# Optimization experiments

Measured on AMD Instinct MI355X. Metric: run time of the kernel, lower is better.

## Reference

```python
import jax, jax.numpy as jnp
import numpy as np

N_NODES = 50000
EMBED_DIM = 512
N_EDGES = 800000
NEG_SLOPE = 0.01  # nn.LeakyReLU default


def setup_inputs() -> dict:
    key = jax.random.key(0)
    k1, k2, k3 = jax.random.split(key, 3)
    X = jax.random.normal(k1, (N_NODES, EMBED_DIM), dtype=jnp.float32)
    # Glorot-ish scale for the GCNConv weight
    W = jax.random.normal(k2, (EMBED_DIM, EMBED_DIM), dtype=jnp.float32) / np.sqrt(EMBED_DIM)
    b = jnp.zeros((EMBED_DIM,), dtype=jnp.float32)
    edge_index = jax.random.randint(k3, (2, N_EDGES), 0, N_NODES, dtype=jnp.int32)
    return {"X": X, "W": W, "b": b, "edge_index": edge_index}


def reference(X, W, b, edge_index):
    N = X.shape[0]
    # GCNConv: add self-loops, symmetric normalization deg^-1/2 A deg^-1/2
    loop = jnp.arange(N, dtype=edge_index.dtype)
    src = jnp.concatenate([edge_index[0], loop])  # [E+N]
    dst = jnp.concatenate([edge_index[1], loop])  # [E+N]
    deg = jax.ops.segment_sum(jnp.ones_like(dst, dtype=X.dtype), dst, num_segments=N)
    dinv = jnp.where(deg > 0, jax.lax.rsqrt(deg), 0.0)  # deg^{-1/2}, inf->0
    norm = dinv[src] * dinv[dst]                         # [E+N]
    H = X @ W                                            # [N, D] dense GEMM
    msgs = H[src] * norm[:, None]                        # [E+N, D] gathered messages
    out = jax.ops.segment_sum(msgs, dst, num_segments=N) + b
    # LeakyReLU activation; Dropout is identity in eval mode
    return jnp.where(out >= 0, out, NEG_SLOPE * out)
```

## Files before the change

kernel.cpp:

```cpp
#include <hip/hip_runtime.h>
#include <cstdint>
#include <cstddef>

#define DFEAT 512
#define BM 128
#define BN 128
#define BK 32

typedef __attribute__((ext_vector_type(8))) short bf16x8;
typedef __attribute__((ext_vector_type(4))) float f32x4;

#define GLOBAL_AS __attribute__((address_space(1)))
#define LDS_AS __attribute__((address_space(3)))

__device__ __forceinline__ unsigned short f2bf(float f) {
  unsigned u = __float_as_uint(f);
  u = u + 0x7fffu + ((u >> 16) & 1u);
  return (unsigned short)(u >> 16);
}

__device__ __forceinline__ float bf2f_lo(unsigned u) { return __uint_as_float(u << 16); }
__device__ __forceinline__ float bf2f_hi(unsigned u) { return __uint_as_float(u & 0xffff0000u); }

__device__ __forceinline__ void gl_lds16(const void* g, void* l) {
  __builtin_amdgcn_global_load_lds((const GLOBAL_AS unsigned int*)g,
                                   (LDS_AS unsigned int*)l, 16, 0, 0);
}

__global__ void k_init(int* __restrict__ deg, int* __restrict__ fill, int N) {
  int i = blockIdx.x * blockDim.x + threadIdx.x;
  if (i < N) { deg[i] = 1; fill[i] = 0; }
}

__global__ void k_count(const int* __restrict__ dst, int* __restrict__ deg, int E) {
  int i = blockIdx.x * blockDim.x + threadIdx.x;
  if (i < E) atomicAdd(&deg[dst[i]], 1);
}

__global__ void k_dinv(const int* __restrict__ deg, float* __restrict__ dinv, int N) {
  int i = blockIdx.x * blockDim.x + threadIdx.x;
  if (i < N) dinv[i] = rsqrtf((float)deg[i]);
}

__global__ void k_scan(const int* __restrict__ deg, int* __restrict__ rowStart, int N) {
  const int t = threadIdx.x;
  const int C = (N + 1023) / 1024;
  int lo = t * C;
  int hi = lo + C; if (hi > N) hi = N; if (lo > N) lo = N;
  int sum = 0;
  for (int i = lo; i < hi; ++i) sum += deg[i];
  __shared__ int sm[1024];
  sm[t] = sum;
  __syncthreads();
  for (int d = 1; d < 1024; d <<= 1) {
    int v = (t >= d) ? sm[t - d] : 0;
    __syncthreads();
    sm[t] += v;
    __syncthreads();
  }
  int off = sm[t] - sum;
  for (int i = lo; i < hi; ++i) { rowStart[i] = off; off += deg[i]; }
  if (t == 1023) rowStart[N] = sm[1023];
}

__global__ void k_fill(const int* __restrict__ src, const int* __restrict__ dst,
                       const int* __restrict__ rowStart, int* __restrict__ fill,
                       int2* __restrict__ cw, const float* __restrict__ dinv, int E, int N) {
  int i = blockIdx.x * blockDim.x + threadIdx.x;
  if (i >= E + N) return;
  int d, s;
  if (i < E) { d = dst[i]; s = src[i]; }
  else       { d = i - E; s = d; }
  int pos = rowStart[d] + atomicAdd(&fill[d], 1);
  int2 q; q.x = s; q.y = __float_as_int(dinv[s]);
  cw[pos] = q;
}

__global__ void k_wt(const float* __restrict__ W, unsigned short* __restrict__ Wt) {
  int i = blockIdx.x * blockDim.x + threadIdx.x;
  int k = i >> 9, n = i & 511;
  Wt[(size_t)n * DFEAT + k] = f2bf(W[i]);
}

__global__ void k_xb(const float* __restrict__ X, unsigned short* __restrict__ Xb, int total8) {
  int i = blockIdx.x * blockDim.x + threadIdx.x;
  if (i >= total8) return;
  const float4 a = *reinterpret_cast<const float4*>(X + (size_t)i * 8);
  const float4 c = *reinterpret_cast<const float4*>(X + (size_t)i * 8 + 4);
  uint4 o;
  o.x = (unsigned)f2bf(a.x) | ((unsigned)f2bf(a.y) << 16);
  o.y = (unsigned)f2bf(a.z) | ((unsigned)f2bf(a.w) << 16);
  o.z = (unsigned)f2bf(c.x) | ((unsigned)f2bf(c.y) << 16);
  o.w = (unsigned)f2bf(c.z) | ((unsigned)f2bf(c.w) << 16);
  *reinterpret_cast<uint4*>(Xb + (size_t)i * 8) = o;
}

__global__ __launch_bounds__(256) void k_aggregate(const unsigned short* __restrict__ Xb,
                                                   const int2* __restrict__ cw,
                                                   const int* __restrict__ rowStart,
                                                   const float* __restrict__ dinv,
                                                   unsigned short* __restrict__ Y, int N) {
  const int row = blockIdx.x * 4 + (threadIdx.x >> 6);
  const int lane = threadIdx.x & 63;
  float acc[8] = {0.f, 0.f, 0.f, 0.f, 0.f, 0.f, 0.f, 0.f};
  if (row < N) {
    const int s = rowStart[row], e = rowStart[row + 1];
    int p = s;
    for (; p + 4 <= e; p += 4) {
      const int2 q0 = cw[p + 0];
      const int2 q1 = cw[p + 1];
      const int2 q2 = cw[p + 2];
      const int2 q3 = cw[p + 3];
      const uint4 v0 = *reinterpret_cast<const uint4*>(Xb + (size_t)q0.x * DFEAT + lane * 8);
      const uint4 v1 = *reinterpret_cast<const uint4*>(Xb + (size_t)q1.x * DFEAT + lane * 8);
      const uint4 v2 = *reinterpret_cast<const uint4*>(Xb + (size_t)q2.x * DFEAT + lane * 8);
      const uint4 v3 = *reinterpret_cast<const uint4*>(Xb + (size_t)q3.x * DFEAT + lane * 8);
      const float w0 = __int_as_float(q0.y), w1 = __int_as_float(q1.y);
      const float w2 = __int_as_float(q2.y), w3 = __int_as_float(q3.y);
      acc[0] = fmaf(w0, bf2f_lo(v0.x), acc[0]); acc[1] = fmaf(w0, bf2f_hi(v0.x), acc[1]);
      acc[2] = fmaf(w0, bf2f_lo(v0.y), acc[2]); acc[3] = fmaf(w0, bf2f_hi(v0.y), acc[3]);
      acc[4] = fmaf(w0, bf2f_lo(v0.z), acc[4]); acc[5] = fmaf(w0, bf2f_hi(v0.z), acc[5]);
      acc[6] = fmaf(w0, bf2f_lo(v0.w), acc[6]); acc[7] = fmaf(w0, bf2f_hi(v0.w), acc[7]);
      acc[0] = fmaf(w1, bf2f_lo(v1.x), acc[0]); acc[1] = fmaf(w1, bf2f_hi(v1.x), acc[1]);
      acc[2] = fmaf(w1, bf2f_lo(v1.y), acc[2]); acc[3] = fmaf(w1, bf2f_hi(v1.y), acc[3]);
      acc[4] = fmaf(w1, bf2f_lo(v1.z), acc[4]); acc[5] = fmaf(w1, bf2f_hi(v1.z), acc[5]);
      acc[6] = fmaf(w1, bf2f_lo(v1.w), acc[6]); acc[7] = fmaf(w1, bf2f_hi(v1.w), acc[7]);
      acc[0] = fmaf(w2, bf2f_lo(v2.x), acc[0]); acc[1] = fmaf(w2, bf2f_hi(v2.x), acc[1]);
      acc[2] = fmaf(w2, bf2f_lo(v2.y), acc[2]); acc[3] = fmaf(w2, bf2f_hi(v2.y), acc[3]);
      acc[4] = fmaf(w2, bf2f_lo(v2.z), acc[4]); acc[5] = fmaf(w2, bf2f_hi(v2.z), acc[5]);
      acc[6] = fmaf(w2, bf2f_lo(v2.w), acc[6]); acc[7] = fmaf(w2, bf2f_hi(v2.w), acc[7]);
      acc[0] = fmaf(w3, bf2f_lo(v3.x), acc[0]); acc[1] = fmaf(w3, bf2f_hi(v3.x), acc[1]);
      acc[2] = fmaf(w3, bf2f_lo(v3.y), acc[2]); acc[3] = fmaf(w3, bf2f_hi(v3.y), acc[3]);
      acc[4] = fmaf(w3, bf2f_lo(v3.z), acc[4]); acc[5] = fmaf(w3, bf2f_hi(v3.z), acc[5]);
      acc[6] = fmaf(w3, bf2f_lo(v3.w), acc[6]); acc[7] = fmaf(w3, bf2f_hi(v3.w), acc[7]);
    }
    for (; p < e; ++p) {
      const int2 q = cw[p];
      const float w = __int_as_float(q.y);
      const uint4 v = *reinterpret_cast<const uint4*>(Xb + (size_t)q.x * DFEAT + lane * 8);
      acc[0] = fmaf(w, bf2f_lo(v.x), acc[0]); acc[1] = fmaf(w, bf2f_hi(v.x), acc[1]);
      acc[2] = fmaf(w, bf2f_lo(v.y), acc[2]); acc[3] = fmaf(w, bf2f_hi(v.y), acc[3]);
      acc[4] = fmaf(w, bf2f_lo(v.z), acc[4]); acc[5] = fmaf(w, bf2f_hi(v.z), acc[5]);
      acc[6] = fmaf(w, bf2f_lo(v.w), acc[6]); acc[7] = fmaf(w, bf2f_hi(v.w), acc[7]);
    }
    const float sc = dinv[row];
#pragma unroll
    for (int j = 0; j < 8; ++j) acc[j] *= sc;
  }
  uint4 o;
  o.x = (unsigned)f2bf(acc[0]) | ((unsigned)f2bf(acc[1]) << 16);
  o.y = (unsigned)f2bf(acc[2]) | ((unsigned)f2bf(acc[3]) << 16);
  o.z = (unsigned)f2bf(acc[4]) | ((unsigned)f2bf(acc[5]) << 16);
  o.w = (unsigned)f2bf(acc[6]) | ((unsigned)f2bf(acc[7]) << 16);
  *reinterpret_cast<uint4*>(Y + (size_t)row * DFEAT + lane * 8) = o;
}

__global__ __launch_bounds__(256) void k_gemm(const unsigned short* __restrict__ Y,
                                              const unsigned short* __restrict__ Wt,
                                              const float* __restrict__ bias,
                                              float* __restrict__ out, int M) {
  __shared__ unsigned short As[BM * BK];
  __shared__ unsigned short Bs[BN * BK];
  const int tid = threadIdx.x;
  const int lane = tid & 63;
  const int wave = tid >> 6;
  const int l16 = lane & 15;
  const int quad = lane >> 4;
  const int wm = (wave >> 1) * 64;
  const int wn = (wave & 1) * 64;
  const int m0 = blockIdx.x * BM;
  const int n0 = blockIdx.y * BN;

  f32x4 acc[4][4];
#pragma unroll
  for (int mi = 0; mi < 4; ++mi)
#pragma unroll
    for (int ni = 0; ni < 4; ++ni) { f32x4 z = {0.f, 0.f, 0.f, 0.f}; acc[mi][ni] = z; }

  const int ci0 = wave * 64 + lane;
  const int ci1 = 256 + ci0;
  const int ra0 = ci0 >> 2, ka0 = (((ci0 & 3) - (ra0 >> 1)) & 3) * 8;
  const int ra1 = ci1 >> 2, ka1 = (((ci1 & 3) - (ra1 >> 1)) & 3) * 8;

  const unsigned short* Ag0 = Y + (size_t)(m0 + ra0) * DFEAT + ka0;
  const unsigned short* Ag1 = Y + (size_t)(m0 + ra1) * DFEAT + ka1;
  const unsigned short* Bg0 = Wt + (size_t)(n0 + ra0) * DFEAT + ka0;
  const unsigned short* Bg1 = Wt + (size_t)(n0 + ra1) * DFEAT + ka1;
  unsigned short* La0 = As + ci0 * 8;
  unsigned short* La1 = As + ci1 * 8;
  unsigned short* Lb0 = Bs + ci0 * 8;
  unsigned short* Lb1 = Bs + ci1 * 8;

  const int rotA = (quad + ((wm + l16) >> 1)) & 3;
  const int rotB = (quad + ((wn + l16) >> 1)) & 3;
  const unsigned short* AsRd = As + (wm + l16) * BK + rotA * 8;
  const unsigned short* BsRd = Bs + (wn + l16) * BK + rotB * 8;

  for (int kk = 0; kk < DFEAT; kk += BK) {
    gl_lds16(Ag0 + kk, La0);
    gl_lds16(Ag1 + kk, La1);
    gl_lds16(Bg0 + kk, Lb0);
    gl_lds16(Bg1 + kk, Lb1);
    __syncthreads();
    bf16x8 av[4], bv[4];
#pragma unroll
    for (int mi = 0; mi < 4; ++mi)
      av[mi] = *reinterpret_cast<const bf16x8*>(AsRd + mi * 16 * BK);
#pragma unroll
    for (int ni = 0; ni < 4; ++ni)
      bv[ni] = *reinterpret_cast<const bf16x8*>(BsRd + ni * 16 * BK);
#pragma unroll
    for (int mi = 0; mi < 4; ++mi)
#pragma unroll
      for (int ni = 0; ni < 4; ++ni)
        acc[mi][ni] = __builtin_amdgcn_mfma_f32_16x16x32_bf16(av[mi], bv[ni], acc[mi][ni], 0, 0, 0);
    __syncthreads();
  }

  float bvals[4];
#pragma unroll
  for (int ni = 0; ni < 4; ++ni) bvals[ni] = bias[n0 + wn + 16 * ni + l16];

#pragma unroll
  for (int mi = 0; mi < 4; ++mi) {
#pragma unroll
    for (int r = 0; r < 4; ++r) {
      int row = m0 + wm + 16 * mi + quad * 4 + r;
      if (row < M) {
#pragma unroll
        for (int ni = 0; ni < 4; ++ni) {
          float v = acc[mi][ni][r] + bvals[ni];
          v = (v >= 0.f) ? v : 0.01f * v;
          out[(size_t)row * DFEAT + n0 + wn + 16 * ni + l16] = v;
        }
      }
    }
  }
}

extern "C" void kernel_launch(void* const* d_in, const int* in_sizes, int n_in,
                              void* d_out, int out_size, void* d_ws, size_t ws_size,
                              hipStream_t stream) {
  const float* X = (const float*)d_in[0];
  const float* W = (const float*)d_in[1];
  const float* b = (const float*)d_in[2];
  const int* ei  = (const int*)d_in[3];
  const int D = DFEAT;
  const int N = in_sizes[0] / D;
  const int E = in_sizes[3] / 2;
  const int* src = ei;
  const int* dst = ei + E;
  float* out = (float*)d_out;

  uintptr_t p = (uintptr_t)d_ws;
  auto carve = [&](size_t bytes) -> void* {
    uintptr_t r = p;
    p += (bytes + 255) & ~(size_t)255;
    return (void*)r;
  };
  int*   deg      = (int*)carve(sizeof(int) * (size_t)N);
  int*   fill     = (int*)carve(sizeof(int) * (size_t)N);
  int*   rowStart = (int*)carve(sizeof(int) * (size_t)(N + 1));
  float* dinv     = (float*)carve(sizeof(float) * (size_t)N);
  int2*  cw       = (int2*)carve(sizeof(int2) * (size_t)(E + N));
  unsigned short* Wt = (unsigned short*)carve(sizeof(unsigned short) * (size_t)D * D);
  const int Mtiles = (N + BM - 1) / BM;
  const int Mpad = Mtiles * BM;
  unsigned short* Y  = (unsigned short*)carve(sizeof(unsigned short) * (size_t)Mpad * D);

  unsigned short* Xb = (unsigned short*)d_out;

  hipLaunchKernelGGL(k_init,  dim3((N + 255) / 256), dim3(256), 0, stream, deg, fill, N);
  hipLaunchKernelGGL(k_count, dim3((E + 255) / 256), dim3(256), 0, stream, dst, deg, E);
  hipLaunchKernelGGL(k_dinv,  dim3((N + 255) / 256), dim3(256), 0, stream, deg, dinv, N);
  hipLaunchKernelGGL(k_scan,  dim3(1), dim3(1024), 0, stream, deg, rowStart, N);
  hipLaunchKernelGGL(k_fill,  dim3((E + N + 255) / 256), dim3(256), 0, stream,
                     src, dst, rowStart, fill, cw, dinv, E, N);
  hipLaunchKernelGGL(k_wt,    dim3((D * D) / 256), dim3(256), 0, stream, W, Wt);
  hipLaunchKernelGGL(k_xb,    dim3((N * D / 8 + 255) / 256), dim3(256), 0, stream,
                     X, Xb, N * D / 8);
  hipLaunchKernelGGL(k_aggregate, dim3(Mpad / 4), dim3(256), 0, stream,
                     Xb, cw, rowStart, dinv, Y, N);
  hipLaunchKernelGGL(k_gemm,  dim3(Mtiles, D / BN), dim3(256), 0, stream, Y, Wt, b, out, N);
}
```

Measured before the change: 508.4 us.

## Unroll aggregation gather to 8 edges and remap GEMM tiles per XCD

The aggregation loop now issues eight row-gather loads before any FMAs, and handles the tail with a clamped, zero-weighted batch instead of a scalar remainder loop. The aim is more memory-level parallelism on the latency-bound gather. The GEMM grid is flattened to 1D and block IDs are remapped so that the blocks landing on one XCD work on contiguous M-tiles, sharing all four N-tiles of each row panel to improve L2 reuse. The price is higher register pressure in the aggregation kernel and some wasted loads in the tail batch.

```diff
diff --git a/kernel.cpp b/kernel.cpp
--- a/kernel.cpp
+++ b/kernel.cpp
@@ -95,6 +95,32 @@
   *reinterpret_cast<uint4*>(Xb + (size_t)i * 8) = o;
 }
 
+template <bool TAIL>
+__device__ __forceinline__ void agg8(const unsigned short* __restrict__ Xb,
+                                     const int2* __restrict__ cw,
+                                     int p, int e, int lane, float* acc) {
+  int2 q[8];
+#pragma unroll
+  for (int i = 0; i < 8; ++i) {
+    int pi = p + i;
+    if (TAIL) pi = (pi < e) ? pi : (e - 1);
+    q[i] = cw[pi];
+  }
+  uint4 v[8];
+#pragma unroll
+  for (int i = 0; i < 8; ++i)
+    v[i] = *reinterpret_cast<const uint4*>(Xb + (size_t)q[i].x * DFEAT + lane * 8);
+#pragma unroll
+  for (int i = 0; i < 8; ++i) {
+    float w = __int_as_float(q[i].y);
+    if (TAIL) w = (p + i < e) ? w : 0.0f;
+    acc[0] = fmaf(w, bf2f_lo(v[i].x), acc[0]); acc[1] = fmaf(w, bf2f_hi(v[i].x), acc[1]);
+    acc[2] = fmaf(w, bf2f_lo(v[i].y), acc[2]); acc[3] = fmaf(w, bf2f_hi(v[i].y), acc[3]);
+    acc[4] = fmaf(w, bf2f_lo(v[i].z), acc[4]); acc[5] = fmaf(w, bf2f_hi(v[i].z), acc[5]);
+    acc[6] = fmaf(w, bf2f_lo(v[i].w), acc[6]); acc[7] = fmaf(w, bf2f_hi(v[i].w), acc[7]);
+  }
+}
+
 __global__ __launch_bounds__(256) void k_aggregate(const unsigned short* __restrict__ Xb,
                                                    const int2* __restrict__ cw,
                                                    const int* __restrict__ rowStart,
@@ -106,43 +132,8 @@
   if (row < N) {
     const int s = rowStart[row], e = rowStart[row + 1];
     int p = s;
-    for (; p + 4 <= e; p += 4) {
-      const int2 q0 = cw[p + 0];
-      const int2 q1 = cw[p + 1];
-      const int2 q2 = cw[p + 2];
-      const int2 q3 = cw[p + 3];
-      const uint4 v0 = *reinterpret_cast<const uint4*>(Xb + (size_t)q0.x * DFEAT + lane * 8);
-      const uint4 v1 = *reinterpret_cast<const uint4*>(Xb + (size_t)q1.x * DFEAT + lane * 8);
-      const uint4 v2 = *reinterpret_cast<const uint4*>(Xb + (size_t)q2.x * DFEAT + lane * 8);
-      const uint4 v3 = *reinterpret_cast<const uint4*>(Xb + (size_t)q3.x * DFEAT + lane * 8);
-      const float w0 = __int_as_float(q0.y), w1 = __int_as_float(q1.y);
-      const float w2 = __int_as_float(q2.y), w3 = __int_as_float(q3.y);
-      acc[0] = fmaf(w0, bf2f_lo(v0.x), acc[0]); acc[1] = fmaf(w0, bf2f_hi(v0.x), acc[1]);
-      acc[2] = fmaf(w0, bf2f_lo(v0.y), acc[2]); acc[3] = fmaf(w0, bf2f_hi(v0.y), acc[3]);
-      acc[4] = fmaf(w0, bf2f_lo(v0.z), acc[4]); acc[5] = fmaf(w0, bf2f_hi(v0.z), acc[5]);
-      acc[6] = fmaf(w0, bf2f_lo(v0.w), acc[6]); acc[7] = fmaf(w0, bf2f_hi(v0.w), acc[7]);
-      acc[0] = fmaf(w1, bf2f_lo(v1.x), acc[0]); acc[1] = fmaf(w1, bf2f_hi(v1.x), acc[1]);
-      acc[2] = fmaf(w1, bf2f_lo(v1.y), acc[2]); acc[3] = fmaf(w1, bf2f_hi(v1.y), acc[3]);
-      acc[4] = fmaf(w1, bf2f_lo(v1.z), acc[4]); acc[5] = fmaf(w1, bf2f_hi(v1.z), acc[5]);
-      acc[6] = fmaf(w1, bf2f_lo(v1.w), acc[6]); acc[7] = fmaf(w1, bf2f_hi(v1.w), acc[7]);
-      acc[0] = fmaf(w2, bf2f_lo(v2.x), acc[0]); acc[1] = fmaf(w2, bf2f_hi(v2.x), acc[1]);
-      acc[2] = fmaf(w2, bf2f_lo(v2.y), acc[2]); acc[3] = fmaf(w2, bf2f_hi(v2.y), acc[3]);
-      acc[4] = fmaf(w2, bf2f_lo(v2.z), acc[4]); acc[5] = fmaf(w2, bf2f_hi(v2.z), acc[5]);
-      acc[6] = fmaf(w2, bf2f_lo(v2.w), acc[6]); acc[7] = fmaf(w2, bf2f_hi(v2.w), acc[7]);
-      acc[0] = fmaf(w3, bf2f_lo(v3.x), acc[0]); acc[1] = fmaf(w3, bf2f_hi(v3.x), acc[1]);
-      acc[2] = fmaf(w3, bf2f_lo(v3.y), acc[2]); acc[3] = fmaf(w3, bf2f_hi(v3.y), acc[3]);
-      acc[4] = fmaf(w3, bf2f_lo(v3.z), acc[4]); acc[5] = fmaf(w3, bf2f_hi(v3.z), acc[5]);
-      acc[6] = fmaf(w3, bf2f_lo(v3.w), acc[6]); acc[7] = fmaf(w3, bf2f_hi(v3.w), acc[7]);
-    }
-    for (; p < e; ++p) {
-      const int2 q = cw[p];
-      const float w = __int_as_float(q.y);
-      const uint4 v = *reinterpret_cast<const uint4*>(Xb + (size_t)q.x * DFEAT + lane * 8);
-      acc[0] = fmaf(w, bf2f_lo(v.x), acc[0]); acc[1] = fmaf(w, bf2f_hi(v.x), acc[1]);
-      acc[2] = fmaf(w, bf2f_lo(v.y), acc[2]); acc[3] = fmaf(w, bf2f_hi(v.y), acc[3]);
-      acc[4] = fmaf(w, bf2f_lo(v.z), acc[4]); acc[5] = fmaf(w, bf2f_hi(v.z), acc[5]);
-      acc[6] = fmaf(w, bf2f_lo(v.w), acc[6]); acc[7] = fmaf(w, bf2f_hi(v.w), acc[7]);
-    }
+    for (; p + 8 <= e; p += 8) agg8<false>(Xb, cw, p, e, lane, acc);
+    if (p < e) agg8<true>(Xb, cw, p, e, lane, acc);
     const float sc = dinv[row];
 #pragma unroll
     for (int j = 0; j < 8; ++j) acc[j] *= sc;
@@ -168,8 +159,13 @@
   const int quad = lane >> 4;
   const int wm = (wave >> 1) * 64;
   const int wn = (wave & 1) * 64;
-  const int m0 = blockIdx.x * BM;
-  const int n0 = blockIdx.y * BN;
+
+  const int nwg = gridDim.x;
+  const int q8 = nwg >> 3, r8 = nwg & 7;
+  const int xcd = blockIdx.x & 7, loc = blockIdx.x >> 3;
+  const int wg = (xcd < r8 ? xcd * (q8 + 1) : r8 * (q8 + 1) + (xcd - r8) * q8) + loc;
+  const int m0 = (wg >> 2) * BM;
+  const int n0 = (wg & 3) * BN;
 
   f32x4 acc[4][4];
 #pragma unroll
@@ -281,5 +277,5 @@
                      X, Xb, N * D / 8);
   hipLaunchKernelGGL(k_aggregate, dim3(Mpad / 4), dim3(256), 0, stream,
                      Xb, cw, rowStart, dinv, Y, N);
-  hipLaunchKernelGGL(k_gemm,  dim3(Mtiles, D / BN), dim3(256), 0, stream, Y, Wt, b, out, N);
-}
+  hipLaunchKernelGGL(k_gemm,  dim3(Mtiles * 4), dim3(256), 0, stream, Y, Wt, b, out, N);
+}
```

New measurement: 501.4 us. Within noise of the previous version (-1.4%).
